# Kernel optimization log

Hardware: AMD Instinct MI355X
Metric: run time of the kernel (lower is better)

Reference implementation:

```python
import jax, jax.numpy as jnp
import numpy as np

D = 1024
LD = 64
NTR = 8192
NT = 8192
DY = 128

def setup_inputs() -> dict:
    key = jax.random.key(0)
    k1, k2, k3, k4 = jax.random.split(key, 4)
    xtr = jax.random.normal(k1, (NTR, D), dtype=jnp.float32)
    ytr = jax.random.normal(k2, (NTR, DY), dtype=jnp.float32)
    xt = jax.random.normal(k3, (NT, D), dtype=jnp.float32)
    A = jax.random.normal(k4, (D, LD), dtype=jnp.float32) / (D ** 0.5)
    return {"xtr": xtr, "ytr": ytr, "xt": xt, "A": A}

def reference(xtr, ytr, xt, A):
    # mean-center both train and test features with the train mean
    mu = jnp.mean(xtr, axis=0, keepdims=True)          # [1, d]
    qtr = (xtr - mu) @ A                                # [Ntr, ld]
    qt = (xt - mu) @ A                                  # [Nt, ld]
    scores = jnp.einsum('nl,ml->nm', qt, qtr)           # [Nt, Ntr]
    E = jax.nn.softmax(scores, axis=1)                  # row-wise softmax over train points
    return E @ ytr                                      # [Nt, dy]
```

## Files before the change

kernel.cpp:

```cpp
#include <hip/hip_runtime.h>
#include <hip/hip_bf16.h>

#define D    1024
#define LD   64
#define NTR  8192
#define NT   8192
#define DY   128

#define SHIFT 40.0f
#define NCHUNK 16
#define CHUNK (NTR / NCHUNK)

typedef __attribute__((ext_vector_type(8))) short bf16x8;
typedef __attribute__((ext_vector_type(8))) _Float16 half8;
typedef __attribute__((ext_vector_type(4))) short short4_;
typedef __attribute__((ext_vector_type(4))) float f4;

static __device__ __forceinline__ short f2bf(float f) {
    __hip_bfloat16 h = __float2bfloat16(f);
    short s; __builtin_memcpy(&s, &h, 2); return s;
}
static __device__ __forceinline__ float bf2f(short s) {
    __hip_bfloat16 h; __builtin_memcpy(&h, &s, 2); return __bfloat162float(h);
}
static __device__ __forceinline__ short f2h(float f) {
    _Float16 h = (_Float16)f;
    short s; __builtin_memcpy(&s, &h, 2); return s;
}
static __device__ __forceinline__ float h2f(short s) {
    _Float16 h; __builtin_memcpy(&h, &s, 2); return (float)h;
}

static __device__ __forceinline__ void gload_lds16(const void* g, void* l) {
    __builtin_amdgcn_global_load_lds(
        (const __attribute__((address_space(1))) unsigned int*)g,
        (__attribute__((address_space(3))) unsigned int*)l,
        16, 0, 0);
}

#define WAIT_VM8() __builtin_amdgcn_s_waitcnt(0x3F78)

__global__ __launch_bounds__(256) void proj_prep(const float* __restrict__ xt,
                                                 const float* __restrict__ xtr,
                                                 const float* __restrict__ A,
                                                 const float* __restrict__ ytr,
                                                 short* __restrict__ qt_hi,
                                                 short* __restrict__ qt_lo,
                                                 short* __restrict__ ktr,
                                                 float* __restrict__ muAp,
                                                 short* __restrict__ vtile) {
    __shared__ __align__(16) float xbuf[4][3][1024];

    int tid = threadIdx.x;
    int b = blockIdx.x;

    if (b >= 256) {
        __shared__ float tile[64][66];
        int bz = b - 256;
        int t0 = (bz & 127) * 64;
        int d0 = (bz >> 7) * 64;
        int c = tid & 63;
        int r4 = tid >> 6;
        #pragma unroll
        for (int i = 0; i < 16; ++i) {
            int r = i * 4 + r4;
            tile[r][c] = ytr[(long)(t0 + r) * DY + d0 + c];
        }
        __syncthreads();
        #pragma unroll
        for (int i = 0; i < 16; ++i) {
            int r = i * 4 + r4;
            int t = t0 + c;
            int dy = d0 + r;
            long idx = (long)(t >> 5) * 4096 + (long)dy * 32
                     + ((((t >> 3) & 3) ^ (dy & 3)) << 3) + (t & 7);
            vtile[idx] = f2bf(tile[c][r]);
        }
        return;
    }

    int wave = tid >> 6;
    int lane = tid & 63;
    int quad = lane >> 4;
    int l16 = lane & 15;

    int g = b * 4 + wave;
    bool is_test = g < (NT / 16);
    int row0 = (is_test ? g : g - NT / 16) * 16;
    const float* x = is_test ? xt : xtr;

    int sr = lane >> 4;
    int cg0 = (lane & 15);

    f4 acc[4];
    #pragma unroll
    for (int ct = 0; ct < 4; ++ct) acc[ct] = (f4){0.f, 0.f, 0.f, 0.f};

    int pr0 = ((quad * 2) ^ (l16 & 7)) * 4;
    int pr1 = (((quad * 2) | 1) ^ (l16 & 7)) * 4;

#define PROJ_DMA(S, BUF)                                                        \
    {                                                                           \
        int kk0 = ((S) & 15) * 64;                                              \
        _Pragma("unroll")                                                       \
        for (int j = 0; j < 4; ++j) {                                           \
            int r = j * 4 + sr;                                                 \
            int cgl = cg0 ^ (r & 7);                                            \
            gload_lds16(x + (long)(row0 + r) * D + kk0 + cgl * 4,               \
                        &xbuf[wave][BUF][j * 256]);                             \
        }                                                                       \
    }

    PROJ_DMA(0, 0)
    PROJ_DMA(1, 1)

    #pragma unroll 1
    for (int s = 0; s < 16; ++s) {
        int cur = s % 3;
        PROJ_DMA(s + 2, (s + 2) % 3)
        WAIT_VM8();

        const float* xrow = &xbuf[wave][cur][l16 * 64];
        bf16x8 ah[2], al[2];
        #pragma unroll
        for (int h = 0; h < 2; ++h) {
            f4 v0 = *(const f4*)(xrow + h * 32 + pr0);
            f4 v1 = *(const f4*)(xrow + h * 32 + pr1);
            #pragma unroll
            for (int e = 0; e < 4; ++e) {
                short hi0 = f2bf(v0[e]);
                short hi1 = f2bf(v1[e]);
                ah[h][e]     = hi0;
                ah[h][e + 4] = hi1;
                al[h][e]     = f2bf(v0[e] - bf2f(hi0));
                al[h][e + 4] = f2bf(v1[e] - bf2f(hi1));
            }
        }

        int k0 = s * 64;
        #pragma unroll
        for (int ct = 0; ct < 4; ++ct) {
            const float* Acol = A + ct * 16 + l16;
            bf16x8 bh0, bh1, bl0, bl1;
            #pragma unroll
            for (int j = 0; j < 8; ++j) {
                float a0 = Acol[(long)(k0 + quad * 8 + j) * LD];
                float a1 = Acol[(long)(k0 + 32 + quad * 8 + j) * LD];
                short h0 = f2bf(a0);
                short h1 = f2bf(a1);
                bh0[j] = h0; bl0[j] = f2bf(a0 - bf2f(h0));
                bh1[j] = h1; bl1[j] = f2bf(a1 - bf2f(h1));
            }
            f4 a = acc[ct];
            a = __builtin_amdgcn_mfma_f32_16x16x32_bf16(ah[0], bh0, a, 0, 0, 0);
            a = __builtin_amdgcn_mfma_f32_16x16x32_bf16(al[0], bh0, a, 0, 0, 0);
            a = __builtin_amdgcn_mfma_f32_16x16x32_bf16(ah[0], bl0, a, 0, 0, 0);
            a = __builtin_amdgcn_mfma_f32_16x16x32_bf16(ah[1], bh1, a, 0, 0, 0);
            a = __builtin_amdgcn_mfma_f32_16x16x32_bf16(al[1], bh1, a, 0, 0, 0);
            a = __builtin_amdgcn_mfma_f32_16x16x32_bf16(ah[1], bl1, a, 0, 0, 0);
            acc[ct] = a;
        }
    }
#undef PROJ_DMA

    #pragma unroll
    for (int ct = 0; ct < 4; ++ct) {
        int col = ct * 16 + l16;
        #pragma unroll
        for (int r = 0; r < 4; ++r) {
            int grow = row0 + quad * 4 + r;
            float qv = acc[ct][r];
            if (is_test) {
                short hi = f2h(qv);
                qt_hi[(long)grow * LD + col] = hi;
                qt_lo[(long)grow * LD + col] = f2h(qv - h2f(hi));
            } else {
                int tl = grow & 31;
                long idx = (long)(grow >> 5) * 2048 + tl * 64
                         + ((((col >> 3) ^ (tl & 7))) << 3) + (col & 7);
                ktr[idx] = f2h(qv);
            }
        }
        if (!is_test) {
            float s = acc[ct][0] + acc[ct][1] + acc[ct][2] + acc[ct][3];
            s += __shfl_xor(s, 16);
            s += __shfl_xor(s, 32);
            if (quad == 0) muAp[(long)(g - NT / 16) * 64 + col] = s;
        }
    }
}

__global__ __launch_bounds__(256) void center_q(short* __restrict__ qt_hi,
                                                short* __restrict__ qt_lo,
                                                const float* __restrict__ muAp) {
    __shared__ float red[4][64];
    __shared__ __align__(16) float muAs[64];
    int l = threadIdx.x & 63;
    int g = threadIdx.x >> 6;
    float ms = 0.f;
    #pragma unroll 8
    for (int p = g; p < 512; p += 4) ms += muAp[(long)p * 64 + l];
    red[g][l] = ms;
    __syncthreads();
    if (threadIdx.x < 64)
        muAs[l] = (red[0][l] + red[1][l] + red[2][l] + red[3][l]) *
                  (1.0f / (float)NTR);
    __syncthreads();

    int t = threadIdx.x;
    int row = t >> 1;
    int ch = (t & 1) * 32;
    long off = (long)blockIdx.x * 128 * LD + (long)row * LD + ch;
    #pragma unroll
    for (int c = 0; c < 4; ++c) {
        bf16x8 hi8 = *(const bf16x8*)&qt_hi[off + c * 8];
        bf16x8 lo8 = *(const bf16x8*)&qt_lo[off + c * 8];
        bf16x8 nh, nl;
        #pragma unroll
        for (int e = 0; e < 8; ++e) {
            float q = h2f(hi8[e]) + h2f(lo8[e]) - muAs[ch + c * 8 + e];
            short hh = f2h(q);
            nh[e] = hh;
            nl[e] = f2h(q - h2f(hh));
        }
        *(bf16x8*)&qt_hi[off + c * 8] = nh;
        *(bf16x8*)&qt_lo[off + c * 8] = nl;
    }
}

__global__ __launch_bounds__(256, 2) void flash_kernel(const short* __restrict__ qt_hi,
                                                       const short* __restrict__ qt_lo,
                                                       const short* __restrict__ ksw,
                                                       const short* __restrict__ vtile,
                                                       short* __restrict__ Opart,
                                                       float* __restrict__ Lpart) {
    __shared__ __align__(16) short kbh[2][2048];
    __shared__ __align__(16) short vbuf[2][4096];
    __shared__ __align__(16) short ptile[4][2560];

    int tid = threadIdx.x;
    int wave = tid >> 6;
    int lane = tid & 63;
    int quad = lane >> 4;
    int l16 = lane & 15;

    int kc = blockIdx.x & 15;
    int qi = blockIdx.x >> 4;
    int q0w = qi * 256 + wave * 64;
    int tile0 = kc * 16;

    int soff = wave * 512 + lane * 8;
    int ldso = wave * 512;

    half8 qh[4][2], ql[4][2];
    #pragma unroll
    for (int rt = 0; rt < 4; ++rt) {
        const short* qrh = qt_hi + (long)(q0w + rt * 16 + l16) * LD + quad * 8;
        const short* qrl = qt_lo + (long)(q0w + rt * 16 + l16) * LD + quad * 8;
        qh[rt][0] = *(const half8*)qrh;
        qh[rt][1] = *(const half8*)(qrh + 32);
        ql[rt][0] = *(const half8*)qrl;
        ql[rt][1] = *(const half8*)(qrl + 32);
    }

    bf16x8 onef;
    #pragma unroll
    for (int i = 0; i < 8; ++i) onef[i] = (short)0x3F80;

    f4 Ov[4][8];
    f4 Lv[4];
    #pragma unroll
    for (int rt = 0; rt < 4; ++rt) {
        Lv[rt] = (f4){0.f, 0.f, 0.f, 0.f};
        #pragma unroll
        for (int jt = 0; jt < 8; ++jt) Ov[rt][jt] = (f4){0.f, 0.f, 0.f, 0.f};
    }

    short* myp = &ptile[wave][0];
    const int p0 = ((quad ^ (l16 & 7)) << 3);
    const int pv = ((quad ^ (l16 & 3)) << 3);

    gload_lds16(ksw + (long)tile0 * 2048 + soff, &kbh[0][ldso]);
    gload_lds16(vtile + (long)tile0 * 4096 + soff, &vbuf[0][ldso]);
    gload_lds16(vtile + (long)tile0 * 4096 + 2048 + soff, &vbuf[0][2048 + ldso]);
    __syncthreads();

    #pragma unroll 1
    for (int it = 0; it < 16; ++it) {
        int cur = it & 1;

        if (it < 15) {
            int nb = cur ^ 1;
            long tb = (long)(tile0 + it + 1);
            gload_lds16(ksw + tb * 2048 + soff, &kbh[nb][ldso]);
            gload_lds16(vtile + tb * 4096 + soff, &vbuf[nb][ldso]);
            gload_lds16(vtile + tb * 4096 + 2048 + soff, &vbuf[nb][2048 + ldso]);
        }

        half8 kh[2][2];
        #pragma unroll
        for (int tt = 0; tt < 2; ++tt) {
            int rb = (tt * 16 + l16) * 64;
            kh[tt][0] = *(const half8*)&kbh[cur][rb + p0];
            kh[tt][1] = *(const half8*)&kbh[cur][rb + (p0 ^ 32)];
        }

        #pragma unroll
        for (int rt = 0; rt < 4; ++rt) {
            #pragma unroll
            for (int tt = 0; tt < 2; ++tt) {
                f4 a = (f4){0.f, 0.f, 0.f, 0.f};
                a = __builtin_amdgcn_mfma_f32_16x16x32_f16(kh[tt][0], qh[rt][0], a, 0, 0, 0);
                a = __builtin_amdgcn_mfma_f32_16x16x32_f16(kh[tt][0], ql[rt][0], a, 0, 0, 0);
                a = __builtin_amdgcn_mfma_f32_16x16x32_f16(kh[tt][1], qh[rt][1], a, 0, 0, 0);
                a = __builtin_amdgcn_mfma_f32_16x16x32_f16(kh[tt][1], ql[rt][1], a, 0, 0, 0);
                short4_ p4;
                p4[0] = f2bf(__expf(a[0] - SHIFT));
                p4[1] = f2bf(__expf(a[1] - SHIFT));
                p4[2] = f2bf(__expf(a[2] - SHIFT));
                p4[3] = f2bf(__expf(a[3] - SHIFT));
                *(short4_*)&myp[(rt * 16 + l16) * 40 + tt * 16 + quad * 4] = p4;
            }
        }

        bf16x8 pf[4];
        #pragma unroll
        for (int rt = 0; rt < 4; ++rt)
            pf[rt] = *(const bf16x8*)&myp[(rt * 16 + l16) * 40 + quad * 8];
        #pragma unroll
        for (int jt = 0; jt < 8; ++jt) {
            bf16x8 vf = *(const bf16x8*)&vbuf[cur][(jt * 16 + l16) * 32 + pv];
            #pragma unroll
            for (int rt = 0; rt < 4; ++rt)
                Ov[rt][jt] = __builtin_amdgcn_mfma_f32_16x16x32_bf16(pf[rt], vf, Ov[rt][jt], 0, 0, 0);
        }
        #pragma unroll
        for (int rt = 0; rt < 4; ++rt)
            Lv[rt] = __builtin_amdgcn_mfma_f32_16x16x32_bf16(pf[rt], onef, Lv[rt], 0, 0, 0);

        __syncthreads();
    }

    long ob = (long)kc * NT;
    #pragma unroll
    for (int rt = 0; rt < 4; ++rt) {
        #pragma unroll
        for (int jt = 0; jt < 8; ++jt) {
            #pragma unroll
            for (int r = 0; r < 4; ++r)
                Opart[(ob + q0w + rt * 16 + quad * 4 + r) * DY + jt * 16 + l16] =
                    f2bf(Ov[rt][jt][r]);
        }
        if (l16 == 0) {
            #pragma unroll
            for (int r = 0; r < 4; ++r)
                Lpart[ob + q0w + rt * 16 + quad * 4 + r] = Lv[rt][r];
        }
    }
}

__global__ __launch_bounds__(256) void finalize_kernel(const short* __restrict__ Opart,
                                                       const float* __restrict__ Lpart,
                                                       float* __restrict__ out) {
    long i = ((long)blockIdx.x * 256 + threadIdx.x) * 8;
    long row = i >> 7;
    float L = 0.f;
    f4 a = (f4){0.f, 0.f, 0.f, 0.f};
    f4 b = (f4){0.f, 0.f, 0.f, 0.f};
    #pragma unroll
    for (int kc = 0; kc < NCHUNK; ++kc) {
        L += Lpart[(long)kc * NT + row];
        bf16x8 o = *(const bf16x8*)&Opart[(long)kc * NT * DY + i];
        #pragma unroll
        for (int j = 0; j < 4; ++j) {
            a[j] += bf2f(o[j]);
            b[j] += bf2f(o[j + 4]);
        }
    }
    float linv = 1.0f / L;
    a *= linv; b *= linv;
    *(f4*)&out[i] = a;
    *(f4*)&out[i + 4] = b;
}

extern "C" void kernel_launch(void* const* d_in, const int* in_sizes, int n_in,
                              void* d_out, int out_size, void* d_ws, size_t ws_size,
                              hipStream_t stream) {
    const float* xtr = (const float*)d_in[0];
    const float* ytr = (const float*)d_in[1];
    const float* xt  = (const float*)d_in[2];
    const float* A   = (const float*)d_in[3];
    float* out = (float*)d_out;

    char* w = (char*)d_ws;
    float* muAp  = (float*)w; w += (size_t)512 * 64 * 4;
    float* Lpart = (float*)w; w += (size_t)NCHUNK * NT * 4;
    short* Opart = (short*)w; w += (size_t)NCHUNK * NT * DY * 2;
    short* qt_hi  = (short*)w; w += (size_t)NT * LD * 2;
    short* qt_lo  = (short*)w; w += (size_t)NT * LD * 2;
    short* ksw    = (short*)w; w += (size_t)NTR * LD * 2;
    short* vtile  = (short*)w; w += (size_t)DY * NTR * 2;
    (void)ws_size; (void)in_sizes; (void)n_in; (void)out_size;

    proj_prep<<<512, 256, 0, stream>>>(xt, xtr, A, ytr,
                                       qt_hi, qt_lo, ksw, muAp, vtile);
    center_q<<<64, 256, 0, stream>>>(qt_hi, qt_lo, muAp);
    flash_kernel<<<512, 256, 0, stream>>>(qt_hi, qt_lo, ksw, vtile,
                                          Opart, Lpart);
    finalize_kernel<<<(NT * DY) / (256 * 8), 256, 0, stream>>>(Opart, Lpart, out);
}
```

Before: 172.2 us.

## Pre-split A into bf16 hi/lo once and fold query centering into flash kernel

Adds a small prep kernel that transposes A and splits it into bf16 hi/lo arrays, so the projection kernel loads ready-made vectors instead of doing strided scalar loads and conversions for every tile. The separate center_q kernel is removed. Each flash block now reduces the mean-projection partials itself and subtracts them while loading its query fragments. The projection kernel also shares one LDS buffer between its two roles. This trades a launch and a global read/write pass over Q for redundant muAp reductions in all 512 flash blocks, plus one extra small launch.

```diff
diff --git a/kernel.cpp b/kernel.cpp
--- a/kernel.cpp
+++ b/kernel.cpp
@@ -40,22 +40,38 @@
 
 #define WAIT_VM8() __builtin_amdgcn_s_waitcnt(0x3F78)
 
+__global__ __launch_bounds__(256) void prep_A(const float* __restrict__ A,
+                                              short* __restrict__ AThi,
+                                              short* __restrict__ ATlo) {
+    int k = blockIdx.x * 16 + (threadIdx.x >> 4);
+    int c0 = (threadIdx.x & 15) * 4;
+    f4 a = *(const f4*)&A[(long)k * LD + c0];
+    #pragma unroll
+    for (int j = 0; j < 4; ++j) {
+        int c = c0 + j;
+        short hi = f2bf(a[j]);
+        AThi[(long)c * D + k] = hi;
+        ATlo[(long)c * D + k] = f2bf(a[j] - bf2f(hi));
+    }
+}
+
 __global__ __launch_bounds__(256) void proj_prep(const float* __restrict__ xt,
                                                  const float* __restrict__ xtr,
-                                                 const float* __restrict__ A,
+                                                 const short* __restrict__ AThi,
+                                                 const short* __restrict__ ATlo,
                                                  const float* __restrict__ ytr,
                                                  short* __restrict__ qt_hi,
                                                  short* __restrict__ qt_lo,
                                                  short* __restrict__ ktr,
                                                  float* __restrict__ muAp,
                                                  short* __restrict__ vtile) {
-    __shared__ __align__(16) float xbuf[4][3][1024];
+    __shared__ __align__(16) float smem[12288];
 
     int tid = threadIdx.x;
     int b = blockIdx.x;
 
     if (b >= 256) {
-        __shared__ float tile[64][66];
+        float (*tile)[66] = (float (*)[66])smem;
         int bz = b - 256;
         int t0 = (bz & 127) * 64;
         int d0 = (bz >> 7) * 64;
@@ -78,6 +94,8 @@
         }
         return;
     }
+
+    float (*xbuf)[3][1024] = (float (*)[3][1024])smem;
 
     int wave = tid >> 6;
     int lane = tid & 63;
@@ -140,17 +158,12 @@
         int k0 = s * 64;
         #pragma unroll
         for (int ct = 0; ct < 4; ++ct) {
-            const float* Acol = A + ct * 16 + l16;
-            bf16x8 bh0, bh1, bl0, bl1;
-            #pragma unroll
-            for (int j = 0; j < 8; ++j) {
-                float a0 = Acol[(long)(k0 + quad * 8 + j) * LD];
-                float a1 = Acol[(long)(k0 + 32 + quad * 8 + j) * LD];
-                short h0 = f2bf(a0);
-                short h1 = f2bf(a1);
-                bh0[j] = h0; bl0[j] = f2bf(a0 - bf2f(h0));
-                bh1[j] = h1; bl1[j] = f2bf(a1 - bf2f(h1));
-            }
+            const short* bh = AThi + (long)(ct * 16 + l16) * D + k0 + quad * 8;
+            const short* bl = ATlo + (long)(ct * 16 + l16) * D + k0 + quad * 8;
+            bf16x8 bh0 = *(const bf16x8*)bh;
+            bf16x8 bh1 = *(const bf16x8*)(bh + 32);
+            bf16x8 bl0 = *(const bf16x8*)bl;
+            bf16x8 bl1 = *(const bf16x8*)(bl + 32);
             f4 a = acc[ct];
             a = __builtin_amdgcn_mfma_f32_16x16x32_bf16(ah[0], bh0, a, 0, 0, 0);
             a = __builtin_amdgcn_mfma_f32_16x16x32_bf16(al[0], bh0, a, 0, 0, 0);
@@ -190,53 +203,18 @@
     }
 }
 
-__global__ __launch_bounds__(256) void center_q(short* __restrict__ qt_hi,
-                                                short* __restrict__ qt_lo,
-                                                const float* __restrict__ muAp) {
-    __shared__ float red[4][64];
-    __shared__ __align__(16) float muAs[64];
-    int l = threadIdx.x & 63;
-    int g = threadIdx.x >> 6;
-    float ms = 0.f;
-    #pragma unroll 8
-    for (int p = g; p < 512; p += 4) ms += muAp[(long)p * 64 + l];
-    red[g][l] = ms;
-    __syncthreads();
-    if (threadIdx.x < 64)
-        muAs[l] = (red[0][l] + red[1][l] + red[2][l] + red[3][l]) *
-                  (1.0f / (float)NTR);
-    __syncthreads();
-
-    int t = threadIdx.x;
-    int row = t >> 1;
-    int ch = (t & 1) * 32;
-    long off = (long)blockIdx.x * 128 * LD + (long)row * LD + ch;
-    #pragma unroll
-    for (int c = 0; c < 4; ++c) {
-        bf16x8 hi8 = *(const bf16x8*)&qt_hi[off + c * 8];
-        bf16x8 lo8 = *(const bf16x8*)&qt_lo[off + c * 8];
-        bf16x8 nh, nl;
-        #pragma unroll
-        for (int e = 0; e < 8; ++e) {
-            float q = h2f(hi8[e]) + h2f(lo8[e]) - muAs[ch + c * 8 + e];
-            short hh = f2h(q);
-            nh[e] = hh;
-            nl[e] = f2h(q - h2f(hh));
-        }
-        *(bf16x8*)&qt_hi[off + c * 8] = nh;
-        *(bf16x8*)&qt_lo[off + c * 8] = nl;
-    }
-}
-
 __global__ __launch_bounds__(256, 2) void flash_kernel(const short* __restrict__ qt_hi,
                                                        const short* __restrict__ qt_lo,
                                                        const short* __restrict__ ksw,
                                                        const short* __restrict__ vtile,
+                                                       const float* __restrict__ muAp,
                                                        short* __restrict__ Opart,
                                                        float* __restrict__ Lpart) {
     __shared__ __align__(16) short kbh[2][2048];
     __shared__ __align__(16) short vbuf[2][4096];
     __shared__ __align__(16) short ptile[4][2560];
+    __shared__ float redm[4][64];
+    __shared__ float muAs[64];
 
     int tid = threadIdx.x;
     int wave = tid >> 6;
@@ -252,38 +230,61 @@
     int soff = wave * 512 + lane * 8;
     int ldso = wave * 512;
 
-    half8 qh[4][2], ql[4][2];
-    #pragma unroll
-    for (int rt = 0; rt < 4; ++rt) {
-        const short* qrh = qt_hi + (long)(q0w + rt * 16 + l16) * LD + quad * 8;
-        const short* qrl = qt_lo + (long)(q0w + rt * 16 + l16) * LD + quad * 8;
-        qh[rt][0] = *(const half8*)qrh;
-        qh[rt][1] = *(const half8*)(qrh + 32);
-        ql[rt][0] = *(const half8*)qrl;
-        ql[rt][1] = *(const half8*)(qrl + 32);
-    }
-
-    bf16x8 onef;
-    #pragma unroll
-    for (int i = 0; i < 8; ++i) onef[i] = (short)0x3F80;
-
-    f4 Ov[4][8];
-    f4 Lv[4];
-    #pragma unroll
-    for (int rt = 0; rt < 4; ++rt) {
-        Lv[rt] = (f4){0.f, 0.f, 0.f, 0.f};
-        #pragma unroll
-        for (int jt = 0; jt < 8; ++jt) Ov[rt][jt] = (f4){0.f, 0.f, 0.f, 0.f};
-    }
-
-    short* myp = &ptile[wave][0];
-    const int p0 = ((quad ^ (l16 & 7)) << 3);
-    const int pv = ((quad ^ (l16 & 3)) << 3);
-
+    {
+        int l = tid & 63;
+        int gg = tid >> 6;
+        float ms = 0.f;
+        #pragma unroll 8
+        for (int p = gg; p < 512; p += 4) ms += muAp[(long)p * 64 + l];
+        redm[gg][l] = ms;
+    }
     gload_lds16(ksw + (long)tile0 * 2048 + soff, &kbh[0][ldso]);
     gload_lds16(vtile + (long)tile0 * 4096 + soff, &vbuf[0][ldso]);
     gload_lds16(vtile + (long)tile0 * 4096 + 2048 + soff, &vbuf[0][2048 + ldso]);
     __syncthreads();
+    if (tid < 64)
+        muAs[tid] = (redm[0][tid] + redm[1][tid] + redm[2][tid] + redm[3][tid]) *
+                    (1.0f / (float)NTR);
+    __syncthreads();
+
+    half8 qh[4][2], ql[4][2];
+    #pragma unroll
+    for (int rt = 0; rt < 4; ++rt) {
+        const short* qrh = qt_hi + (long)(q0w + rt * 16 + l16) * LD + quad * 8;
+        const short* qrl = qt_lo + (long)(q0w + rt * 16 + l16) * LD + quad * 8;
+        #pragma unroll
+        for (int h = 0; h < 2; ++h) {
+            bf16x8 hbits = *(const bf16x8*)(qrh + h * 32);
+            bf16x8 lbits = *(const bf16x8*)(qrl + h * 32);
+            half8 nh, nl;
+            #pragma unroll
+            for (int e = 0; e < 8; ++e) {
+                float qc = h2f(hbits[e]) + h2f(lbits[e]) - muAs[h * 32 + quad * 8 + e];
+                _Float16 hh = (_Float16)qc;
+                nh[e] = hh;
+                nl[e] = (_Float16)(qc - (float)hh);
+            }
+            qh[rt][h] = nh;
+            ql[rt][h] = nl;
+        }
+    }
+
+    bf16x8 onef;
+    #pragma unroll
+    for (int i = 0; i < 8; ++i) onef[i] = (short)0x3F80;
+
+    f4 Ov[4][8];
+    f4 Lv[4];
+    #pragma unroll
+    for (int rt = 0; rt < 4; ++rt) {
+        Lv[rt] = (f4){0.f, 0.f, 0.f, 0.f};
+        #pragma unroll
+        for (int jt = 0; jt < 8; ++jt) Ov[rt][jt] = (f4){0.f, 0.f, 0.f, 0.f};
+    }
+
+    short* myp = &ptile[wave][0];
+    const int p0 = ((quad ^ (l16 & 7)) << 3);
+    const int pv = ((quad ^ (l16 & 3)) << 3);
 
     #pragma unroll 1
     for (int it = 0; it < 16; ++it) {
@@ -396,16 +397,18 @@
     float* muAp  = (float*)w; w += (size_t)512 * 64 * 4;
     float* Lpart = (float*)w; w += (size_t)NCHUNK * NT * 4;
     short* Opart = (short*)w; w += (size_t)NCHUNK * NT * DY * 2;
+    short* AThi  = (short*)w; w += (size_t)LD * D * 2;
+    short* ATlo  = (short*)w; w += (size_t)LD * D * 2;
     short* qt_hi  = (short*)w; w += (size_t)NT * LD * 2;
     short* qt_lo  = (short*)w; w += (size_t)NT * LD * 2;
     short* ksw    = (short*)w; w += (size_t)NTR * LD * 2;
     short* vtile  = (short*)w; w += (size_t)DY * NTR * 2;
     (void)ws_size; (void)in_sizes; (void)n_in; (void)out_size;
 
-    proj_prep<<<512, 256, 0, stream>>>(xt, xtr, A, ytr,
+    prep_A<<<64, 256, 0, stream>>>(A, AThi, ATlo);
+    proj_prep<<<512, 256, 0, stream>>>(xt, xtr, AThi, ATlo, ytr,
                                        qt_hi, qt_lo, ksw, muAp, vtile);
-    center_q<<<64, 256, 0, stream>>>(qt_hi, qt_lo, muAp);
-    flash_kernel<<<512, 256, 0, stream>>>(qt_hi, qt_lo, ksw, vtile,
+    flash_kernel<<<512, 256, 0, stream>>>(qt_hi, qt_lo, ksw, vtile, muAp,
                                           Opart, Lpart);
     finalize_kernel<<<(NT * DY) / (256 * 8), 256, 0, stream>>>(Opart, Lpart, out);
 }
```

After: 181.6 us. 5.4% more time.
